# Kernel tuning notes

Hardware: AMD Instinct MI355X
Metric: run time of the kernel (lower is better)

The kernel has to match this reference:

```python
import jax, jax.numpy as jnp
import numpy as np

N, E, B = 25000, 400000, 64
IN, HID, OUT, EDGE, TDIM, L = 16, 128, 16, 16, 64, 4
EIN = 2 * HID + 1 + EDGE  # 273


def _sinusoidal(t, dim):
    half = dim // 2
    freqs = jnp.exp(jnp.arange(half, dtype=jnp.float32) * (-np.log(10000.0) / (half - 1)))
    a = t[:, None] * freqs[None, :]
    return jnp.concatenate([jnp.sin(a), jnp.cos(a)], axis=-1)


def _layernorm(h, g, b, eps=1e-5):
    mu = h.mean(-1, keepdims=True)
    v = h.var(-1, keepdims=True)
    return (h - mu) / jnp.sqrt(v + eps) * g + b


def setup_inputs() -> dict:
    key = jax.random.key(0)
    ks = iter(jax.random.split(key, 64))

    def rn(shape, scale=0.05):
        return jax.random.normal(next(ks), shape, dtype=jnp.float32) * scale

    inp = {
        'h': jax.random.normal(next(ks), (N, IN), dtype=jnp.float32),
        'x': jax.random.normal(next(ks), (N, 3), dtype=jnp.float32),
        'edge_index': jax.random.randint(next(ks), (2, E), 0, N),
        't': jax.random.uniform(next(ks), (B,), dtype=jnp.float32) * 1000.0,
        'edge_attr': jax.random.normal(next(ks), (E, EDGE), dtype=jnp.float32),
        'batch': jnp.sort(jax.random.randint(next(ks), (N,), 0, B)),
        # embeddings
        'node_w': rn((IN, HID)), 'node_b': jnp.zeros((HID,), jnp.float32),
        'tw1': rn((TDIM, HID)), 'tb1': jnp.zeros((HID,), jnp.float32),
        'tw2': rn((HID, HID)), 'tb2': jnp.zeros((HID,), jnp.float32),
        # per-layer stacked params (L, ...)
        'edge_w1': rn((L, EIN, HID)), 'edge_b1': jnp.zeros((L, HID), jnp.float32),
        'edge_w2': rn((L, HID, HID)), 'edge_b2': jnp.zeros((L, HID), jnp.float32),
        'att_w': rn((L, HID, 1)), 'att_b': jnp.zeros((L, 1), jnp.float32),
        'cw1': rn((L, HID, HID)), 'cb1': jnp.zeros((L, HID), jnp.float32),
        'cw2': rn((L, HID, 1), scale=0.001),  # xavier gain=0.001
        'nw1': rn((L, 2 * HID, HID)), 'nb1': jnp.zeros((L, HID), jnp.float32),
        'nw2': rn((L, HID, HID)), 'nb2': jnp.zeros((L, HID), jnp.float32),
        'ln_g': jnp.ones((L, HID), jnp.float32), 'ln_b': jnp.zeros((L, HID), jnp.float32),
        # heads
        'out_w1': rn((HID, HID)), 'out_b1': jnp.zeros((HID,), jnp.float32),
        'out_w2': rn((HID, OUT)), 'out_b2': jnp.zeros((OUT,), jnp.float32),
        'head_w': rn((HID, 3), scale=0.01), 'head_b': jnp.zeros((3,), jnp.float32),
    }
    return inp


def reference(h, x, edge_index, t, edge_attr, batch,
              node_w, node_b, tw1, tb1, tw2, tb2,
              edge_w1, edge_b1, edge_w2, edge_b2, att_w, att_b,
              cw1, cb1, cw2, nw1, nb1, nw2, nb2, ln_g, ln_b,
              out_w1, out_b1, out_w2, out_b2, head_w, head_b):
    silu = jax.nn.silu
    n_nodes = h.shape[0]
    row, col = edge_index[0], edge_index[1]

    # node + time embedding
    h = h @ node_w + node_b
    te = _sinusoidal(t, TDIM)
    te = silu(te @ tw1 + tb1) @ tw2 + tb2
    h = h + te[batch]

    for i in range(L):
        coord_diff = x[row] - x[col]                      # (E, 3)
        radial = (coord_diff ** 2).sum(-1, keepdims=True)  # (E, 1)
        edge_in = jnp.concatenate([h[row], h[col], radial, edge_attr], axis=-1)
        m = silu(silu(edge_in @ edge_w1[i] + edge_b1[i]) @ edge_w2[i] + edge_b2[i])
        att = jax.nn.sigmoid(m @ att_w[i] + att_b[i])
        m = m * att
        cw = silu(m @ cw1[i] + cb1[i]) @ cw2[i]           # (E, 1)
        coord_diff = coord_diff / jnp.sqrt(radial + 1e-8)  # normalize=True
        x = x + jax.ops.segment_sum(coord_diff * cw, row, num_segments=n_nodes)
        m_i = jax.ops.segment_sum(m, row, num_segments=n_nodes)
        h_in = jnp.concatenate([h, m_i], axis=-1)
        h_new = h + (silu(h_in @ nw1[i] + nb1[i]) @ nw2[i] + nb2[i])
        h = _layernorm(h_new, ln_g[i], ln_b[i])

    h_out = silu(h @ out_w1 + out_b1) @ out_w2 + out_b2  # (N, OUT)
    x_out = h @ head_w + head_b                           # (N, 3)
    return h_out, x_out
```

## Files before the change

### kernel.cpp

```cpp
#include <hip/hip_runtime.h>
#include <hip/hip_bf16.h>
#include <cmath>

#define NN      25000
#define NEDGE   400000
#define NBATCH  64
#define IN_DIM  16
#define HID     128
#define OUT_DIM 16
#define EDGE_DIM 16
#define TDIM    64
#define NL      4
#define EIN     273
#define EPB     64
#define W1KB    36
#define W2KB    16
#define A_PAD   65
#define A3OFF   (16*A_PAD*8)
#define NPB     32
#define NPAD    33

typedef short bfrag __attribute__((ext_vector_type(8)));
typedef float ffrag __attribute__((ext_vector_type(4)));

__device__ __forceinline__ float siluf(float v) { return v / (1.f + __expf(-v)); }
__device__ __forceinline__ float sigm(float v)  { return 1.f / (1.f + __expf(-v)); }
__device__ __forceinline__ unsigned short f2b(float f) {
    unsigned u = __float_as_uint(f);
    u = (u + 0x7FFFu + ((u >> 16) & 1u)) >> 16;
    return (unsigned short)u;
}
__device__ __forceinline__ float b2f(unsigned short b) {
    return __uint_as_float(((unsigned)b) << 16);
}
__device__ __forceinline__ int ileave(int n) {
    return (n & 0x60) | ((n & 15) << 1) | ((n >> 4) & 1);
}

__global__ __launch_bounds__(256) void hist_kernel(const int* __restrict__ row, int* __restrict__ deg) {
    const int tid = blockIdx.x * 256 + threadIdx.x;
    if (tid < NEDGE) atomicAdd(&deg[row[tid]], 1);
}

__global__ __launch_bounds__(1024) void scan_kernel(const int* __restrict__ deg, int* __restrict__ row_start) {
    __shared__ int part[1024];
    const int tid = threadIdx.x;
    const int base = tid * 25;
    int sum = 0;
    for (int i = 0; i < 25; i++) { const int idx = base + i; if (idx < NN) sum += deg[idx]; }
    part[tid] = sum;
    __syncthreads();
    for (int off = 1; off < 1024; off <<= 1) {
        int v = (tid >= off) ? part[tid - off] : 0;
        __syncthreads();
        part[tid] += v;
        __syncthreads();
    }
    int run = part[tid] - sum;
    for (int i = 0; i < 25; i++) {
        const int idx = base + i;
        if (idx < NN) { row_start[idx] = run; run += deg[idx]; }
    }
    if (tid == 1023) row_start[NN] = part[1023];
}

__global__ __launch_bounds__(256) void scatter_kernel(
    const int* __restrict__ row, const int* __restrict__ col,
    const int* __restrict__ row_start, int* __restrict__ cursor,
    int* __restrict__ rowp, int* __restrict__ colp, int* __restrict__ eorder)
{
    const int tid = blockIdx.x * 256 + threadIdx.x;
    if (tid >= NEDGE) return;
    const int r = row[tid];
    const int pos = row_start[r] + atomicAdd(&cursor[r], 1);
    rowp[pos] = r; colp[pos] = col[tid]; eorder[pos] = tid;
}

__global__ __launch_bounds__(256) void ea_pack(
    const float* __restrict__ ea, const int* __restrict__ eorder, unsigned short* __restrict__ eabp)
{
    const int tid = blockIdx.x * 256 + threadIdx.x;
    if (tid >= NEDGE) return;
    const int e = eorder[tid];
    const float4* src = (const float4*)&ea[(size_t)e * 16];
    bfrag o0, o1;
    #pragma unroll
    for (int q = 0; q < 2; q++) {
        const float4 a = src[q];
        o0[q*4+0] = (short)f2b(a.x); o0[q*4+1] = (short)f2b(a.y);
        o0[q*4+2] = (short)f2b(a.z); o0[q*4+3] = (short)f2b(a.w);
    }
    #pragma unroll
    for (int q = 0; q < 2; q++) {
        const float4 a = src[2+q];
        o1[q*4+0] = (short)f2b(a.x); o1[q*4+1] = (short)f2b(a.y);
        o1[q*4+2] = (short)f2b(a.z); o1[q*4+3] = (short)f2b(a.w);
    }
    *(bfrag*)&eabp[(size_t)tid * 16]     = o0;
    *(bfrag*)&eabp[(size_t)tid * 16 + 8] = o1;
}

__global__ __launch_bounds__(256) void prep_w(
    const float* __restrict__ ew1, const float* __restrict__ ew2, const float* __restrict__ cw1,
    unsigned short* __restrict__ w1p, unsigned short* __restrict__ w2p, unsigned short* __restrict__ c1p)
{
    const int PER_L = 68 * 128;
    int tid = blockIdx.x * 256 + threadIdx.x;
    if (tid >= NL * PER_L) return;
    const int l = tid / PER_L, rem = tid % PER_L;
    const int kb = rem >> 7, n = rem & 127;
    unsigned short o[8];
    if (kb < W1KB) {
        const float* W = ew1 + (size_t)l * EIN * HID;
        const int nc = ileave(n);
        #pragma unroll
        for (int j = 0; j < 8; j++) {
            const int k = kb * 8 + j;
            const int ok = (k < 256) ? k : (k < 272 ? k + 1 : (k == 272 ? 256 : -1));
            o[j] = (ok >= 0) ? f2b(W[(size_t)ok * HID + nc]) : (unsigned short)0;
        }
        #pragma unroll
        for (int j = 0; j < 8; j++) w1p[(((size_t)l * W1KB + kb) * 128 + n) * 8 + j] = o[j];
    } else if (kb < W1KB + W2KB) {
        const int kb2 = kb - W1KB;
        const float* W = ew2 + (size_t)l * HID * HID;
        const int nc = ileave(n);
        #pragma unroll
        for (int j = 0; j < 8; j++) o[j] = f2b(W[(size_t)(kb2 * 8 + j) * HID + nc]);
        #pragma unroll
        for (int j = 0; j < 8; j++) w2p[(((size_t)l * W2KB + kb2) * 128 + n) * 8 + j] = o[j];
    } else {
        const int kb2 = kb - W1KB - W2KB;
        const float* W = cw1 + (size_t)l * HID * HID;
        #pragma unroll
        for (int j = 0; j < 8; j++) o[j] = f2b(W[(size_t)(kb2 * 8 + j) * HID + n]);
        #pragma unroll
        for (int j = 0; j < 8; j++) c1p[(((size_t)l * W2KB + kb2) * 128 + n) * 8 + j] = o[j];
    }
}

__global__ __launch_bounds__(256) void prep_w2(
    const float* __restrict__ nw1, const float* __restrict__ nw2,
    const float* __restrict__ ow1, const float* __restrict__ ow2,
    unsigned short* __restrict__ n1p, unsigned short* __restrict__ n2p,
    unsigned short* __restrict__ o1p, unsigned short* __restrict__ o2p)
{
    const int C1 = NL * 32 * 128;
    const int C2 = C1 + NL * 16 * 128;
    const int C3 = C2 + 16 * 128;
    const int C4 = C3 + 16 * 16;
    int tid = blockIdx.x * 256 + threadIdx.x;
    if (tid >= C4) return;
    if (tid < C1) {
        const int l = tid / (32*128), rem = tid % (32*128);
        const int kb = rem >> 7, n = rem & 127;
        const int nc = ileave(n);
        #pragma unroll
        for (int j = 0; j < 8; j++)
            n1p[(size_t)tid*8 + j] = f2b(nw1[((size_t)l*256 + kb*8 + j)*128 + nc]);
    } else if (tid < C2) {
        const int t2 = tid - C1;
        const int l = t2 / (16*128), rem = t2 % (16*128);
        const int kb = rem >> 7, n = rem & 127;
        const int nc = ileave(n);
        #pragma unroll
        for (int j = 0; j < 8; j++)
            n2p[(size_t)t2*8 + j] = f2b(nw2[((size_t)l*128 + kb*8 + j)*128 + nc]);
    } else if (tid < C3) {
        const int t2 = tid - C2;
        const int kb = t2 >> 7, n = t2 & 127;
        #pragma unroll
        for (int j = 0; j < 8; j++)
            o1p[(size_t)t2*8 + j] = f2b(ow1[(size_t)(kb*8 + j)*128 + n]);
    } else {
        const int t2 = tid - C3;
        const int kb = t2 >> 4, n = t2 & 15;
        #pragma unroll
        for (int j = 0; j < 8; j++)
            o2p[(size_t)t2*8 + j] = f2b(ow2[(size_t)(kb*8 + j)*16 + n]);
    }
}

__global__ __launch_bounds__(HID) void te_kernel(
    const float* __restrict__ t, const float* __restrict__ tw1, const float* __restrict__ tb1,
    const float* __restrict__ tw2, const float* __restrict__ tb2, float* __restrict__ te_out)
{
    __shared__ float s0[TDIM];
    __shared__ float s1[HID];
    const int b = blockIdx.x, j = threadIdx.x;
    const float tv = t[b];
    if (j < TDIM) {
        const int k = j & 31;
        const float freq = expf((float)k * (-logf(10000.f) / 31.f));
        const float a = tv * freq;
        s0[j] = (j < 32) ? sinf(a) : cosf(a);
    }
    __syncthreads();
    float acc = tb1[j];
    for (int k = 0; k < TDIM; k++) acc += s0[k] * tw1[k*HID + j];
    s1[j] = siluf(acc);
    __syncthreads();
    float acc2 = tb2[j];
    for (int k = 0; k < HID; k++) acc2 += s1[k] * tw2[k*HID + j];
    te_out[b*HID + j] = acc2;
}

__global__ __launch_bounds__(HID) void embed_kernel(
    const float* __restrict__ h_in, const float* __restrict__ x_in,
    const int* __restrict__ batch,
    const float* __restrict__ node_w, const float* __restrict__ node_b,
    const float* __restrict__ te, float* __restrict__ h, unsigned short* __restrict__ hbf,
    float* __restrict__ x0)
{
    __shared__ float hs[IN_DIM];
    const int n = blockIdx.x, j = threadIdx.x;
    if (j < IN_DIM) hs[j] = h_in[n*IN_DIM + j];
    if (j >= 64 && j < 67) x0[n*3 + (j - 64)] = x_in[n*3 + (j - 64)];
    __syncthreads();
    float acc = node_b[j];
    #pragma unroll
    for (int k = 0; k < IN_DIM; k++) acc += hs[k] * node_w[k*HID + j];
    acc += te[batch[n]*HID + j];
    h[n*HID + j]   = acc;
    hbf[n*HID + j] = f2b(acc);
}

__global__ __launch_bounds__(256) void edge_mfma(
    const unsigned short* __restrict__ hbf, const float* __restrict__ x,
    float* __restrict__ x_new, float* __restrict__ m_i,
    const int* __restrict__ rowp, const int* __restrict__ colp,
    const unsigned short* __restrict__ eabp,
    const unsigned short* __restrict__ W1p, const float* __restrict__ B1,
    const unsigned short* __restrict__ W2p, const float* __restrict__ B2,
    const unsigned short* __restrict__ C1p, const float* __restrict__ CB1,
    const float* __restrict__ AW, const float* __restrict__ ABv,
    const float* __restrict__ CW2)
{
    __shared__ unsigned short sA[W1KB * A_PAD * 8];
    __shared__ int rc[EPB][2];
    __shared__ float AWs[HID];
    float* scr   = (float*)sA;
    float* attS  = scr;
    float* cpart = scr + 64;

    const int t = threadIdx.x;
    const int e0 = blockIdx.x * EPB;
    const int lane = t & 63, w = t >> 6;
    const int quad = lane >> 4, colid = lane & 15;

    float cd0 = 0.f, cd1 = 0.f, cd2 = 0.f;
    if (t < EPB) {
        const int r = rowp[e0 + t], c = colp[e0 + t];
        rc[t][0] = r; rc[t][1] = c;
        const float dx = x[r*3+0] - x[c*3+0];
        const float dy = x[r*3+1] - x[c*3+1];
        const float dz = x[r*3+2] - x[c*3+2];
        const float rad = dx*dx + dy*dy + dz*dz;
        const float inv = 1.f / sqrtf(rad + 1e-8f);
        cd0 = dx*inv; cd1 = dy*inv; cd2 = dz*inv;
        unsigned short* p34 = &sA[(34*A_PAD + t) * 8];
        p34[0] = f2b(rad);
        #pragma unroll
        for (int j = 1; j < 8; j++) p34[j] = 0;
        unsigned short* p35 = &sA[(35*A_PAD + t) * 8];
        #pragma unroll
        for (int j = 0; j < 8; j++) p35[j] = 0;
    }
    if (t >= 128 && t < 256) AWs[t - 128] = AW[t - 128];
    if (t < 128) {
        const int e = t >> 1, hh = t & 1;
        *(bfrag*)&sA[((32 + hh)*A_PAD + e) * 8] = *(const bfrag*)&eabp[(size_t)(e0 + e) * 16 + hh * 8];
    }
    __syncthreads();
    #pragma unroll
    for (int it = 0; it < 8; it++) {
        const int c = t + it * 256;
        const int e = (c >> 4) & 63;
        const int half = c >> 10;
        const int kb16 = c & 15;
        const int node = rc[e][half];
        *(bfrag*)&sA[((half*16 + kb16)*A_PAD + e) * 8] = *(const bfrag*)&hbf[(size_t)node * HID + kb16 * 8];
    }
    __syncthreads();

    ffrag acc1[4][2] = {};
    for (int ks = 0; ks < 9; ks++) {
        const int kb = ks * 4 + quad;
        const bfrag b0 = *(const bfrag*)&W1p[((size_t)kb * 128 + w*32 + colid) * 8];
        const bfrag b1 = *(const bfrag*)&W1p[((size_t)kb * 128 + w*32 + 16 + colid) * 8];
        #pragma unroll
        for (int mt = 0; mt < 4; mt++) {
            const bfrag a = *(const bfrag*)&sA[(kb*A_PAD + mt*16 + colid) * 8];
            acc1[mt][0] = __builtin_amdgcn_mfma_f32_16x16x32_bf16(a, b0, acc1[mt][0], 0, 0, 0);
            acc1[mt][1] = __builtin_amdgcn_mfma_f32_16x16x32_bf16(a, b1, acc1[mt][1], 0, 0, 0);
        }
    }
    __syncthreads();
    {
        const int f0 = w*32 + 2*colid;
        const int kb = f0 >> 3, j = f0 & 7;
        const float b0v = B1[f0], b1v = B1[f0+1];
        #pragma unroll
        for (int mt = 0; mt < 4; mt++)
            #pragma unroll
            for (int reg = 0; reg < 4; reg++) {
                const float v0 = siluf(acc1[mt][0][reg] + b0v);
                const float v1 = siluf(acc1[mt][1][reg] + b1v);
                const int e = mt*16 + quad*4 + reg;
                *(__hip_bfloat162*)&sA[(kb*A_PAD + e) * 8 + j] =
                    __float22bfloat162_rn(make_float2(v0, v1));
            }
    }
    __syncthreads();

    ffrag acc2[4][2] = {};
    for (int ks = 0; ks < 4; ks++) {
        const int kb = ks * 4 + quad;
        const bfrag b0 = *(const bfrag*)&W2p[((size_t)kb * 128 + w*32 + colid) * 8];
        const bfrag b1 = *(const bfrag*)&W2p[((size_t)kb * 128 + w*32 + 16 + colid) * 8];
        #pragma unroll
        for (int mt = 0; mt < 4; mt++) {
            const bfrag a = *(const bfrag*)&sA[(kb*A_PAD + mt*16 + colid) * 8];
            acc2[mt][0] = __builtin_amdgcn_mfma_f32_16x16x32_bf16(a, b0, acc2[mt][0], 0, 0, 0);
            acc2[mt][1] = __builtin_amdgcn_mfma_f32_16x16x32_bf16(a, b1, acc2[mt][1], 0, 0, 0);
        }
    }
    {
        const int f0 = w*32 + 2*colid;
        const int kb = f0 >> 3, j = f0 & 7;
        const float b0v = B2[f0], b1v = B2[f0+1];
        #pragma unroll
        for (int mt = 0; mt < 4; mt++)
            #pragma unroll
            for (int reg = 0; reg < 4; reg++) {
                const float v0 = siluf(acc2[mt][0][reg] + b0v);
                const float v1 = siluf(acc2[mt][1][reg] + b1v);
                const int e = mt*16 + quad*4 + reg;
                *(__hip_bfloat162*)&sA[A3OFF + (kb*A_PAD + e) * 8 + j] =
                    __float22bfloat162_rn(make_float2(v0, v1));
            }
    }
    __syncthreads();

    {
        const int e = t >> 2, q = t & 3;
        float s = 0.f;
        #pragma unroll
        for (int kk = 0; kk < 4; kk++) {
            const int kb = q*4 + kk;
            const bfrag v = *(const bfrag*)&sA[A3OFF + (kb*A_PAD + e) * 8];
            #pragma unroll
            for (int j = 0; j < 8; j++) s += b2f((unsigned short)v[j]) * AWs[kb*8 + j];
        }
        s += __shfl_xor(s, 1);
        s += __shfl_xor(s, 2);
        if (q == 0) attS[e] = sigm(s + ABv[0]);
    }
    __syncthreads();

    ffrag acc3[4][2] = {};
    for (int ks = 0; ks < 4; ks++) {
        const int kb = ks * 4 + quad;
        const bfrag b0 = *(const bfrag*)&C1p[((size_t)kb * 128 + w*32 + colid) * 8];
        const bfrag b1 = *(const bfrag*)&C1p[((size_t)kb * 128 + w*32 + 16 + colid) * 8];
        #pragma unroll
        for (int mt = 0; mt < 4; mt++) {
            const bfrag a = *(const bfrag*)&sA[A3OFF + (kb*A_PAD + mt*16 + colid) * 8];
            acc3[mt][0] = __builtin_amdgcn_mfma_f32_16x16x32_bf16(a, b0, acc3[mt][0], 0, 0, 0);
            acc3[mt][1] = __builtin_amdgcn_mfma_f32_16x16x32_bf16(a, b1, acc3[mt][1], 0, 0, 0);
        }
    }

    {
        const int fkb0 = lane >> 3,     fj = lane & 7;
        const int fkb1 = 8 + (lane >> 3);
        float a0 = 0.f, a1 = 0.f;
        for (int i = 0; i < 16; i++) {
            const int e = (w << 4) + i;
            const float av = attS[e];
            const int r = rc[e][0];
            a0 += b2f(sA[A3OFF + (fkb0*A_PAD + e) * 8 + fj]) * av;
            a1 += b2f(sA[A3OFF + (fkb1*A_PAD + e) * 8 + fj]) * av;
            const bool flush = (i == 15) || (rc[e+1][0] != r);
            if (flush) {
                atomicAdd(&m_i[(size_t)r * HID + lane],      a0);
                atomicAdd(&m_i[(size_t)r * HID + lane + 64], a1);
                a0 = 0.f; a1 = 0.f;
            }
        }
    }

    {
        const float cb0v = CB1[w*32 + colid], cb1v = CB1[w*32 + 16 + colid];
        const float cwv0 = CW2[w*32 + colid], cwv1 = CW2[w*32 + 16 + colid];
        float att_r[4][4];
        #pragma unroll
        for (int mt = 0; mt < 4; mt++) {
            const float4 a4 = *(const float4*)&attS[mt*16 + quad*4];
            att_r[mt][0] = a4.x; att_r[mt][1] = a4.y; att_r[mt][2] = a4.z; att_r[mt][3] = a4.w;
        }
        float p[4][4];
        #pragma unroll
        for (int mt = 0; mt < 4; mt++)
            #pragma unroll
            for (int reg = 0; reg < 4; reg++) p[mt][reg] = 0.f;
        #pragma unroll
        for (int mt = 0; mt < 4; mt++)
            #pragma unroll
            for (int nt = 0; nt < 2; nt++) {
                const float cb = nt ? cb1v : cb0v;
                const float cw = nt ? cwv1 : cwv0;
                #pragma unroll
                for (int reg = 0; reg < 4; reg++)
                    p[mt][reg] += siluf(att_r[mt][reg] * acc3[mt][nt][reg] + cb) * cw;
            }
        __syncthreads();
        #pragma unroll
        for (int mt = 0; mt < 4; mt++)
            #pragma unroll
            for (int reg = 0; reg < 4; reg++) {
                float s = p[mt][reg];
                s += __shfl_xor(s, 1);
                s += __shfl_xor(s, 2);
                s += __shfl_xor(s, 4);
                s += __shfl_xor(s, 8);
                if (colid == 0) cpart[(mt*16 + quad*4 + reg) * 4 + w] = s;
            }
    }
    __syncthreads();
    if (t < EPB) {
        const float s = cpart[t*4+0] + cpart[t*4+1] + cpart[t*4+2] + cpart[t*4+3];
        const int r = rc[t][0];
        atomicAdd(&x_new[r*3+0], cd0 * s);
        atomicAdd(&x_new[r*3+1], cd1 * s);
        atomicAdd(&x_new[r*3+2], cd2 * s);
    }
}

__global__ __launch_bounds__(256) void node_mfma(
    float* __restrict__ h, unsigned short* __restrict__ hbf, const float* __restrict__ m_i,
    const unsigned short* __restrict__ N1p, const float* __restrict__ NB1,
    const unsigned short* __restrict__ N2p, const float* __restrict__ NB2,
    const float* __restrict__ LG, const float* __restrict__ LB)
{
    __shared__ unsigned short sA[32 * NPAD * 8];
    __shared__ float mu_s[NPB], rs_s[NPB];
    float* hres = (float*)sA;

    const int t = threadIdx.x, lane = t & 63, w = t >> 6;
    const int quad = lane >> 4, colid = lane & 15;
    const int n0 = blockIdx.x * NPB;

    #pragma unroll
    for (int it = 0; it < 2; it++) {
        const int c = t + it * 256;
        const int e = c >> 4, kb = c & 15;
        const int nidx = min(n0 + e, NN - 1);
        *(bfrag*)&sA[(kb*NPAD + e) * 8] = *(const bfrag*)&hbf[(size_t)nidx * HID + kb * 8];
    }
    #pragma unroll
    for (int it = 0; it < 2; it++) {
        const int c = t + it * 256;
        const int e = c >> 4, kb = c & 15;
        const int nidx = min(n0 + e, NN - 1);
        const float4 v0 = *(const float4*)&m_i[(size_t)nidx * HID + kb * 8];
        const float4 v1 = *(const float4*)&m_i[(size_t)nidx * HID + kb * 8 + 4];
        bfrag bv;
        bv[0]=(short)f2b(v0.x); bv[1]=(short)f2b(v0.y); bv[2]=(short)f2b(v0.z); bv[3]=(short)f2b(v0.w);
        bv[4]=(short)f2b(v1.x); bv[5]=(short)f2b(v1.y); bv[6]=(short)f2b(v1.z); bv[7]=(short)f2b(v1.w);
        *(bfrag*)&sA[((16 + kb)*NPAD + e) * 8] = bv;
    }
    __syncthreads();

    ffrag acc1[2][2] = {};
    for (int ks = 0; ks < 8; ks++) {
        const int kb = ks * 4 + quad;
        const bfrag b0 = *(const bfrag*)&N1p[((size_t)kb * 128 + w*32 + colid) * 8];
        const bfrag b1 = *(const bfrag*)&N1p[((size_t)kb * 128 + w*32 + 16 + colid) * 8];
        #pragma unroll
        for (int mt = 0; mt < 2; mt++) {
            const bfrag a = *(const bfrag*)&sA[(kb*NPAD + mt*16 + colid) * 8];
            acc1[mt][0] = __builtin_amdgcn_mfma_f32_16x16x32_bf16(a, b0, acc1[mt][0], 0, 0, 0);
            acc1[mt][1] = __builtin_amdgcn_mfma_f32_16x16x32_bf16(a, b1, acc1[mt][1], 0, 0, 0);
        }
    }
    __syncthreads();
    {
        const int f0 = w*32 + 2*colid;
        const int kb = f0 >> 3, j = f0 & 7;
        const float b0v = NB1[f0], b1v = NB1[f0+1];
        #pragma unroll
        for (int mt = 0; mt < 2; mt++)
            #pragma unroll
            for (int reg = 0; reg < 4; reg++) {
                const float v0 = siluf(acc1[mt][0][reg] + b0v);
                const float v1 = siluf(acc1[mt][1][reg] + b1v);
                const int e = mt*16 + quad*4 + reg;
                *(__hip_bfloat162*)&sA[(kb*NPAD + e) * 8 + j] =
                    __float22bfloat162_rn(make_float2(v0, v1));
            }
    }
    __syncthreads();

    ffrag acc2[2][2] = {};
    for (int ks = 0; ks < 4; ks++) {
        const int kb = ks * 4 + quad;
        const bfrag b0 = *(const bfrag*)&N2p[((size_t)kb * 128 + w*32 + colid) * 8];
        const bfrag b1 = *(const bfrag*)&N2p[((size_t)kb * 128 + w*32 + 16 + colid) * 8];
        #pragma unroll
        for (int mt = 0; mt < 2; mt++) {
            const bfrag a = *(const bfrag*)&sA[(kb*NPAD + mt*16 + colid) * 8];
            acc2[mt][0] = __builtin_amdgcn_mfma_f32_16x16x32_bf16(a, b0, acc2[mt][0], 0, 0, 0);
            acc2[mt][1] = __builtin_amdgcn_mfma_f32_16x16x32_bf16(a, b1, acc2[mt][1], 0, 0, 0);
        }
    }
    __syncthreads();
    {
        const int f0 = w*32 + 2*colid;
        const float b0v = NB2[f0], b1v = NB2[f0+1];
        #pragma unroll
        for (int mt = 0; mt < 2; mt++)
            #pragma unroll
            for (int reg = 0; reg < 4; reg++) {
                const int row = mt*16 + quad*4 + reg;
                const int nidx = min(n0 + row, NN - 1);
                const float2 hr = *(const float2*)&h[(size_t)nidx*HID + f0];
                float2 o;
                o.x = acc2[mt][0][reg] + b0v + hr.x;
                o.y = acc2[mt][1][reg] + b1v + hr.y;
                *(float2*)&hres[row*130 + f0] = o;
            }
    }
    __syncthreads();
    {
        const int row = t >> 3, q = t & 7;
        float s = 0.f, s2 = 0.f;
        #pragma unroll
        for (int i = 0; i < 16; i++) {
            const float v = hres[row*130 + q*16 + i];
            s += v; s2 += v*v;
        }
        s += __shfl_xor(s, 1); s2 += __shfl_xor(s2, 1);
        s += __shfl_xor(s, 2); s2 += __shfl_xor(s2, 2);
        s += __shfl_xor(s, 4); s2 += __shfl_xor(s2, 4);
        if (q == 0) {
            const float mu = s * (1.f/HID);
            mu_s[row] = mu;
            rs_s[row] = rsqrtf(s2 * (1.f/HID) - mu*mu + 1e-5f);
        }
    }
    __syncthreads();
    for (int idx = t; idx < NPB*HID; idx += 256) {
        const int row = idx >> 7, f = idx & 127;
        const int n = n0 + row;
        if (n < NN) {
            const float v = (hres[row*130 + f] - mu_s[row]) * rs_s[row] * LG[f] + LB[f];
            h[(size_t)n*HID + f]   = v;
            hbf[(size_t)n*HID + f] = f2b(v);
        }
    }
}

__global__ __launch_bounds__(256) void out_mfma(
    const unsigned short* __restrict__ hbf,
    const unsigned short* __restrict__ O1p, const float* __restrict__ OB1,
    const unsigned short* __restrict__ O2p, const float* __restrict__ OB2,
    const float* __restrict__ HW, const float* __restrict__ HB,
    float* __restrict__ out)
{
    __shared__ unsigned short sA[32 * A_PAD * 8];
    __shared__ float hws[HID*3];
    const int A2O = 16 * A_PAD * 8;

    const int t = threadIdx.x, lane = t & 63, w = t >> 6;
    const int quad = lane >> 4, colid = lane & 15;
    const int n0 = blockIdx.x * 64;

    if (t < 128)      { hws[t] = HW[t]; hws[t+128] = HW[t+128]; }
    else if (t < 256) { const int i = t - 128 + 256; if (i < 384) hws[i] = HW[i]; }
    #pragma unroll
    for (int it = 0; it < 4; it++) {
        const int c = t + it * 256;
        const int e = c >> 4, kb = c & 15;
        const int nidx = min(n0 + e, NN - 1);
        *(bfrag*)&sA[(kb*A_PAD + e) * 8] = *(const bfrag*)&hbf[(size_t)nidx * HID + kb * 8];
    }
    __syncthreads();

    ffrag acc1[4][2] = {};
    for (int ks = 0; ks < 4; ks++) {
        const int kb = ks * 4 + quad;
        const bfrag b0 = *(const bfrag*)&O1p[((size_t)kb * 128 + w*32 + colid) * 8];
        const bfrag b1 = *(const bfrag*)&O1p[((size_t)kb * 128 + w*32 + 16 + colid) * 8];
        #pragma unroll
        for (int mt = 0; mt < 4; mt++) {
            const bfrag a = *(const bfrag*)&sA[(kb*A_PAD + mt*16 + colid) * 8];
            acc1[mt][0] = __builtin_amdgcn_mfma_f32_16x16x32_bf16(a, b0, acc1[mt][0], 0, 0, 0);
            acc1[mt][1] = __builtin_amdgcn_mfma_f32_16x16x32_bf16(a, b1, acc1[mt][1], 0, 0, 0);
        }
    }
    {
        const float bias0 = OB1[w*32 + colid], bias1 = OB1[w*32 + 16 + colid];
        #pragma unroll
        for (int mt = 0; mt < 4; mt++)
            #pragma unroll
            for (int nt = 0; nt < 2; nt++) {
                const float bb = nt ? bias1 : bias0;
                const int f = w*32 + nt*16 + colid;
                const int kb = f >> 3, j = f & 7;
                #pragma unroll
                for (int reg = 0; reg < 4; reg++) {
                    const float v = siluf(acc1[mt][nt][reg] + bb);
                    const int e = mt*16 + quad*4 + reg;
                    sA[A2O + (kb*A_PAD + e) * 8 + j] = f2b(v);
                }
            }
    }
    __syncthreads();

    ffrag acco = {};
    for (int ks = 0; ks < 4; ks++) {
        const int kb = ks * 4 + quad;
        const bfrag a = *(const bfrag*)&sA[A2O + (kb*A_PAD + w*16 + colid) * 8];
        const bfrag b = *(const bfrag*)&O2p[((size_t)kb * 16 + colid) * 8];
        acco = __builtin_amdgcn_mfma_f32_16x16x32_bf16(a, b, acco, 0, 0, 0);
    }
    #pragma unroll
    for (int reg = 0; reg < 4; reg++) {
        const int rowg = w*16 + quad*4 + reg;
        const int n = n0 + rowg;
        if (n < NN) out[(size_t)n*OUT_DIM + colid] = acco[reg] + OB2[colid];
    }

    {
        const int rloc = t >> 2, q = t & 3;
        float s0 = 0.f, s1 = 0.f, s2 = 0.f;
        #pragma unroll
        for (int kk = 0; kk < 4; kk++) {
            const int kb = q*4 + kk;
            const bfrag v = *(const bfrag*)&sA[(kb*A_PAD + rloc) * 8];
            #pragma unroll
            for (int j = 0; j < 8; j++) {
                const float hv = b2f((unsigned short)v[j]);
                const int k = kb*8 + j;
                s0 += hv * hws[k*3+0]; s1 += hv * hws[k*3+1]; s2 += hv * hws[k*3+2];
            }
        }
        s0 += __shfl_xor(s0, 1); s1 += __shfl_xor(s1, 1); s2 += __shfl_xor(s2, 1);
        s0 += __shfl_xor(s0, 2); s1 += __shfl_xor(s1, 2); s2 += __shfl_xor(s2, 2);
        const int n = n0 + rloc;
        if (q == 0 && n < NN) {
            out[(size_t)NN*OUT_DIM + n*3 + 0] = s0 + HB[0];
            out[(size_t)NN*OUT_DIM + n*3 + 1] = s1 + HB[1];
            out[(size_t)NN*OUT_DIM + n*3 + 2] = s2 + HB[2];
        }
    }
}

extern "C" void kernel_launch(void* const* d_in, const int* in_sizes, int n_in,
                              void* d_out, int out_size, void* d_ws, size_t ws_size,
                              hipStream_t stream) {
    (void)in_sizes; (void)n_in; (void)out_size; (void)ws_size;
    const float* h_in      = (const float*)d_in[0];
    const float* x_in      = (const float*)d_in[1];
    const int*   edge_idx  = (const int*)  d_in[2];
    const float* t         = (const float*)d_in[3];
    const float* edge_attr = (const float*)d_in[4];
    const int*   batch     = (const int*)  d_in[5];
    const float* node_w = (const float*)d_in[6];
    const float* node_b = (const float*)d_in[7];
    const float* tw1    = (const float*)d_in[8];
    const float* tb1    = (const float*)d_in[9];
    const float* tw2    = (const float*)d_in[10];
    const float* tb2    = (const float*)d_in[11];
    const float* ew1    = (const float*)d_in[12];
    const float* eb1    = (const float*)d_in[13];
    const float* ew2    = (const float*)d_in[14];
    const float* eb2    = (const float*)d_in[15];
    const float* attw   = (const float*)d_in[16];
    const float* attb   = (const float*)d_in[17];
    const float* cw1    = (const float*)d_in[18];
    const float* cb1    = (const float*)d_in[19];
    const float* cw2    = (const float*)d_in[20];
    const float* nw1    = (const float*)d_in[21];
    const float* nb1    = (const float*)d_in[22];
    const float* nw2    = (const float*)d_in[23];
    const float* nb2    = (const float*)d_in[24];
    const float* lng    = (const float*)d_in[25];
    const float* lnb    = (const float*)d_in[26];
    const float* ow1    = (const float*)d_in[27];
    const float* ob1    = (const float*)d_in[28];
    const float* ow2    = (const float*)d_in[29];
    const float* ob2    = (const float*)d_in[30];
    const float* hw     = (const float*)d_in[31];
    const float* hb     = (const float*)d_in[32];

    const int* row = edge_idx;
    const int* col = edge_idx + NEDGE;

    float* ws  = (float*)d_ws;
    float* te  = ws;
    float* h   = te  + NBATCH*HID;
    float* m_i = h   + (size_t)NN*HID;
    float* x0  = m_i + (size_t)NN*HID;
    float* x1  = x0  + NN*3;
    unsigned short* hbf  = (unsigned short*)(x1 + NN*3);
    unsigned short* eabp = hbf + (size_t)NN*HID;
    unsigned short* w1p  = eabp + (size_t)NEDGE*EDGE_DIM;
    unsigned short* w2p  = w1p + (size_t)NL*W1KB*128*8;
    unsigned short* c1p  = w2p + (size_t)NL*W2KB*128*8;
    unsigned short* n1p  = c1p + (size_t)NL*W2KB*128*8;
    unsigned short* n2p  = n1p + (size_t)NL*32*128*8;
    unsigned short* o1p  = n2p + (size_t)NL*16*128*8;
    unsigned short* o2p  = o1p + (size_t)16*128*8;
    int* deg       = (int*)(o2p + 16*16*8);
    int* row_start = deg + NN;
    int* cursor    = row_start + NN + 1;
    int* rowp      = cursor + NN;
    int* colp      = rowp + NEDGE;
    int* eorder    = colp + NEDGE;

    hipMemsetAsync(deg, 0, NN*sizeof(int), stream);
    hipMemsetAsync(cursor, 0, NN*sizeof(int), stream);
    hist_kernel<<<(NEDGE+255)/256, 256, 0, stream>>>(row, deg);
    scan_kernel<<<1, 1024, 0, stream>>>(deg, row_start);
    scatter_kernel<<<(NEDGE+255)/256, 256, 0, stream>>>(row, col, row_start, cursor, rowp, colp, eorder);
    ea_pack<<<(NEDGE+255)/256, 256, 0, stream>>>(edge_attr, eorder, eabp);

    prep_w<<<(NL*68*128 + 255)/256, 256, 0, stream>>>(ew1, ew2, cw1, w1p, w2p, c1p);
    prep_w2<<<(NL*32*128 + NL*16*128 + 16*128 + 16*16 + 255)/256, 256, 0, stream>>>(
        nw1, nw2, ow1, ow2, n1p, n2p, o1p, o2p);
    te_kernel<<<NBATCH, HID, 0, stream>>>(t, tw1, tb1, tw2, tb2, te);
    embed_kernel<<<NN, HID, 0, stream>>>(h_in, x_in, batch, node_w, node_b, te, h, hbf, x0);

    const int NBLK = (NN + NPB - 1) / NPB;
    const int OBLK = (NN + 63) / 64;
    float* xc = x0; float* xn = x1;
    for (int i = 0; i < NL; i++) {
        hipMemsetAsync(m_i, 0, (size_t)NN*HID*sizeof(float), stream);
        hipMemcpyAsync(xn, xc, (size_t)NN*3*sizeof(float), hipMemcpyDeviceToDevice, stream);
        edge_mfma<<<NEDGE/EPB, 256, 0, stream>>>(
            hbf, xc, xn, m_i, rowp, colp, eabp,
            w1p + (size_t)i*W1KB*128*8, eb1 + (size_t)i*HID,
            w2p + (size_t)i*W2KB*128*8, eb2 + (size_t)i*HID,
            c1p + (size_t)i*W2KB*128*8, cb1 + (size_t)i*HID,
            attw + (size_t)i*HID, attb + i,
            cw2 + (size_t)i*HID);
        node_mfma<<<NBLK, 256, 0, stream>>>(
            h, hbf, m_i,
            n1p + (size_t)i*32*128*8, nb1 + (size_t)i*HID,
            n2p + (size_t)i*16*128*8, nb2 + (size_t)i*HID,
            lng + (size_t)i*HID,      lnb + (size_t)i*HID);
        float* tmp = xc; xc = xn; xn = tmp;
    }

    out_mfma<<<OBLK, 256, 0, stream>>>(hbf, o1p, ob1, o2p, ob2, hw, hb, (float*)d_out);
}
```

Before: 1.083 ms.

## Fold biases into MFMA accumulators, compute attention via MFMA, fuse m_i zeroing

```diff
diff --git a/kernel.cpp b/kernel.cpp
--- a/kernel.cpp
+++ b/kernel.cpp
@@ -102,9 +102,11 @@
 
 __global__ __launch_bounds__(256) void prep_w(
     const float* __restrict__ ew1, const float* __restrict__ ew2, const float* __restrict__ cw1,
-    unsigned short* __restrict__ w1p, unsigned short* __restrict__ w2p, unsigned short* __restrict__ c1p)
-{
-    const int PER_L = 68 * 128;
+    const float* __restrict__ attw,
+    unsigned short* __restrict__ w1p, unsigned short* __restrict__ w2p,
+    unsigned short* __restrict__ c1p, unsigned short* __restrict__ awp)
+{
+    const int PER_L = 70 * 128;
     int tid = blockIdx.x * 256 + threadIdx.x;
     if (tid >= NL * PER_L) return;
     const int l = tid / PER_L, rem = tid % PER_L;
@@ -129,13 +131,22 @@
         for (int j = 0; j < 8; j++) o[j] = f2b(W[(size_t)(kb2 * 8 + j) * HID + nc]);
         #pragma unroll
         for (int j = 0; j < 8; j++) w2p[(((size_t)l * W2KB + kb2) * 128 + n) * 8 + j] = o[j];
-    } else {
+    } else if (kb < W1KB + 2*W2KB) {
         const int kb2 = kb - W1KB - W2KB;
         const float* W = cw1 + (size_t)l * HID * HID;
         #pragma unroll
         for (int j = 0; j < 8; j++) o[j] = f2b(W[(size_t)(kb2 * 8 + j) * HID + n]);
         #pragma unroll
         for (int j = 0; j < 8; j++) c1p[(((size_t)l * W2KB + kb2) * 128 + n) * 8 + j] = o[j];
+    } else {
+        const int kbp = kb - W1KB - 2*W2KB;
+        const int kbA = kbp * 8 + (n >> 4);
+        const int colv = n & 15;
+        const float* AWl = attw + (size_t)l * HID;
+        #pragma unroll
+        for (int j = 0; j < 8; j++) o[j] = f2b(AWl[kbA*8 + j]);
+        #pragma unroll
+        for (int j = 0; j < 8; j++) awp[(((size_t)l * 16 + kbA) * 16 + colv) * 8 + j] = o[j];
     }
 }
 
@@ -205,24 +216,27 @@
     te_out[b*HID + j] = acc2;
 }
 
-__global__ __launch_bounds__(HID) void embed_kernel(
+__global__ __launch_bounds__(256) void embed_kernel(
     const float* __restrict__ h_in, const float* __restrict__ x_in,
     const int* __restrict__ batch,
     const float* __restrict__ node_w, const float* __restrict__ node_b,
     const float* __restrict__ te, float* __restrict__ h, unsigned short* __restrict__ hbf,
-    float* __restrict__ x0)
-{
-    __shared__ float hs[IN_DIM];
-    const int n = blockIdx.x, j = threadIdx.x;
-    if (j < IN_DIM) hs[j] = h_in[n*IN_DIM + j];
+    float* __restrict__ x0, float* __restrict__ m_i)
+{
+    __shared__ float hs[2][IN_DIM];
+    const int local = threadIdx.x >> 7;
+    const int j = threadIdx.x & 127;
+    const int n = blockIdx.x * 2 + local;
+    if (j < IN_DIM) hs[local][j] = h_in[n*IN_DIM + j];
     if (j >= 64 && j < 67) x0[n*3 + (j - 64)] = x_in[n*3 + (j - 64)];
     __syncthreads();
     float acc = node_b[j];
     #pragma unroll
-    for (int k = 0; k < IN_DIM; k++) acc += hs[k] * node_w[k*HID + j];
+    for (int k = 0; k < IN_DIM; k++) acc += hs[local][k] * node_w[k*HID + j];
     acc += te[batch[n]*HID + j];
-    h[n*HID + j]   = acc;
-    hbf[n*HID + j] = f2b(acc);
+    h[(size_t)n*HID + j]   = acc;
+    hbf[(size_t)n*HID + j] = f2b(acc);
+    m_i[(size_t)n*HID + j] = 0.f;
 }
 
 __global__ __launch_bounds__(256) void edge_mfma(
@@ -233,15 +247,13 @@
     const unsigned short* __restrict__ W1p, const float* __restrict__ B1,
     const unsigned short* __restrict__ W2p, const float* __restrict__ B2,
     const unsigned short* __restrict__ C1p, const float* __restrict__ CB1,
-    const float* __restrict__ AW, const float* __restrict__ ABv,
+    const unsigned short* __restrict__ AWp, const float* __restrict__ ABv,
     const float* __restrict__ CW2)
 {
     __shared__ unsigned short sA[W1KB * A_PAD * 8];
     __shared__ int rc[EPB][2];
-    __shared__ float AWs[HID];
-    float* scr   = (float*)sA;
-    float* attS  = scr;
-    float* cpart = scr + 64;
+    float* attS = (float*)sA;
+    float* pscr = (float*)&sA[A3OFF];
 
     const int t = threadIdx.x;
     const int e0 = blockIdx.x * EPB;
@@ -266,7 +278,6 @@
         #pragma unroll
         for (int j = 0; j < 8; j++) p35[j] = 0;
     }
-    if (t >= 128 && t < 256) AWs[t - 128] = AW[t - 128];
     if (t < 128) {
         const int e = t >> 1, hh = t & 1;
         *(bfrag*)&sA[((32 + hh)*A_PAD + e) * 8] = *(const bfrag*)&eabp[(size_t)(e0 + e) * 16 + hh * 8];
@@ -283,7 +294,15 @@
     }
     __syncthreads();
 
-    ffrag acc1[4][2] = {};
+    const int f0 = w*32 + 2*colid;
+    ffrag acc1[4][2];
+    {
+        const float b0v = B1[f0], b1v = B1[f0+1];
+        #pragma unroll
+        for (int mt = 0; mt < 4; mt++)
+            #pragma unroll
+            for (int r = 0; r < 4; r++) { acc1[mt][0][r] = b0v; acc1[mt][1][r] = b1v; }
+    }
     for (int ks = 0; ks < 9; ks++) {
         const int kb = ks * 4 + quad;
         const bfrag b0 = *(const bfrag*)&W1p[((size_t)kb * 128 + w*32 + colid) * 8];
@@ -297,15 +316,13 @@
     }
     __syncthreads();
     {
-        const int f0 = w*32 + 2*colid;
         const int kb = f0 >> 3, j = f0 & 7;
-        const float b0v = B1[f0], b1v = B1[f0+1];
         #pragma unroll
         for (int mt = 0; mt < 4; mt++)
             #pragma unroll
             for (int reg = 0; reg < 4; reg++) {
-                const float v0 = siluf(acc1[mt][0][reg] + b0v);
-                const float v1 = siluf(acc1[mt][1][reg] + b1v);
+                const float v0 = siluf(acc1[mt][0][reg]);
+                const float v1 = siluf(acc1[mt][1][reg]);
                 const int e = mt*16 + quad*4 + reg;
                 *(__hip_bfloat162*)&sA[(kb*A_PAD + e) * 8 + j] =
                     __float22bfloat162_rn(make_float2(v0, v1));
@@ -313,7 +330,14 @@
     }
     __syncthreads();
 
-    ffrag acc2[4][2] = {};
+    ffrag acc2[4][2];
+    {
+        const float b0v = B2[f0], b1v = B2[f0+1];
+        #pragma unroll
+        for (int mt = 0; mt < 4; mt++)
+            #pragma unroll
+            for (int r = 0; r < 4; r++) { acc2[mt][0][r] = b0v; acc2[mt][1][r] = b1v; }
+    }
     for (int ks = 0; ks < 4; ks++) {
         const int kb = ks * 4 + quad;
         const bfrag b0 = *(const bfrag*)&W2p[((size_t)kb * 128 + w*32 + colid) * 8];
@@ -326,15 +350,13 @@
         }
     }
     {
-        const int f0 = w*32 + 2*colid;
         const int kb = f0 >> 3, j = f0 & 7;
-        const float b0v = B2[f0], b1v = B2[f0+1];
         #pragma unroll
         for (int mt = 0; mt < 4; mt++)
             #pragma unroll
             for (int reg = 0; reg < 4; reg++) {
-                const float v0 = siluf(acc2[mt][0][reg] + b0v);
-                const float v1 = siluf(acc2[mt][1][reg] + b1v);
+                const float v0 = siluf(acc2[mt][0][reg]);
+                const float v1 = siluf(acc2[mt][1][reg]);
                 const int e = mt*16 + quad*4 + reg;
                 *(__hip_bfloat162*)&sA[A3OFF + (kb*A_PAD + e) * 8 + j] =
                     __float22bfloat162_rn(make_float2(v0, v1));
@@ -342,34 +364,35 @@
     }
     __syncthreads();
 
-    {
-        const int e = t >> 2, q = t & 3;
-        float s = 0.f;
-        #pragma unroll
-        for (int kk = 0; kk < 4; kk++) {
-            const int kb = q*4 + kk;
-            const bfrag v = *(const bfrag*)&sA[A3OFF + (kb*A_PAD + e) * 8];
-            #pragma unroll
-            for (int j = 0; j < 8; j++) s += b2f((unsigned short)v[j]) * AWs[kb*8 + j];
-        }
-        s += __shfl_xor(s, 1);
-        s += __shfl_xor(s, 2);
-        if (q == 0) attS[e] = sigm(s + ABv[0]);
-    }
-    __syncthreads();
-
+    ffrag accA;
+    {
+        const float abv = ABv[0];
+        #pragma unroll
+        for (int r = 0; r < 4; r++) accA[r] = abv;
+    }
     ffrag acc3[4][2] = {};
     for (int ks = 0; ks < 4; ks++) {
         const int kb = ks * 4 + quad;
-        const bfrag b0 = *(const bfrag*)&C1p[((size_t)kb * 128 + w*32 + colid) * 8];
-        const bfrag b1 = *(const bfrag*)&C1p[((size_t)kb * 128 + w*32 + 16 + colid) * 8];
+        const bfrag ab = *(const bfrag*)&AWp[((size_t)kb * 16 + colid) * 8];
+        const bfrag c0 = *(const bfrag*)&C1p[((size_t)kb * 128 + w*32 + colid) * 8];
+        const bfrag c1 = *(const bfrag*)&C1p[((size_t)kb * 128 + w*32 + 16 + colid) * 8];
+        const bfrag aw_frag = *(const bfrag*)&sA[A3OFF + (kb*A_PAD + w*16 + colid) * 8];
+        accA = __builtin_amdgcn_mfma_f32_16x16x32_bf16(aw_frag, ab, accA, 0, 0, 0);
         #pragma unroll
         for (int mt = 0; mt < 4; mt++) {
-            const bfrag a = *(const bfrag*)&sA[A3OFF + (kb*A_PAD + mt*16 + colid) * 8];
-            acc3[mt][0] = __builtin_amdgcn_mfma_f32_16x16x32_bf16(a, b0, acc3[mt][0], 0, 0, 0);
-            acc3[mt][1] = __builtin_amdgcn_mfma_f32_16x16x32_bf16(a, b1, acc3[mt][1], 0, 0, 0);
-        }
-    }
+            const bfrag a = (mt == w) ? aw_frag
+                : *(const bfrag*)&sA[A3OFF + (kb*A_PAD + mt*16 + colid) * 8];
+            acc3[mt][0] = __builtin_amdgcn_mfma_f32_16x16x32_bf16(a, c0, acc3[mt][0], 0, 0, 0);
+            acc3[mt][1] = __builtin_amdgcn_mfma_f32_16x16x32_bf16(a, c1, acc3[mt][1], 0, 0, 0);
+        }
+    }
+    if (colid == 0) {
+        #pragma unroll
+        for (int reg = 0; reg < 4; reg++) attS[w*16 + quad*4 + reg] = accA[reg];
+    }
+    __syncthreads();
+    if (t < EPB) attS[t] = sigm(attS[t]);
+    __syncthreads();
 
     {
         const int fkb0 = lane >> 3,     fj = lane & 7;
@@ -390,46 +413,35 @@
         }
     }
 
+    float p[4][4];
     {
         const float cb0v = CB1[w*32 + colid], cb1v = CB1[w*32 + 16 + colid];
         const float cwv0 = CW2[w*32 + colid], cwv1 = CW2[w*32 + 16 + colid];
-        float att_r[4][4];
         #pragma unroll
         for (int mt = 0; mt < 4; mt++) {
             const float4 a4 = *(const float4*)&attS[mt*16 + quad*4];
-            att_r[mt][0] = a4.x; att_r[mt][1] = a4.y; att_r[mt][2] = a4.z; att_r[mt][3] = a4.w;
-        }
-        float p[4][4];
-        #pragma unroll
-        for (int mt = 0; mt < 4; mt++)
-            #pragma unroll
-            for (int reg = 0; reg < 4; reg++) p[mt][reg] = 0.f;
-        #pragma unroll
-        for (int mt = 0; mt < 4; mt++)
-            #pragma unroll
-            for (int nt = 0; nt < 2; nt++) {
-                const float cb = nt ? cb1v : cb0v;
-                const float cw = nt ? cwv1 : cwv0;
-                #pragma unroll
-                for (int reg = 0; reg < 4; reg++)
-                    p[mt][reg] += siluf(att_r[mt][reg] * acc3[mt][nt][reg] + cb) * cw;
-            }
-        __syncthreads();
-        #pragma unroll
-        for (int mt = 0; mt < 4; mt++)
-            #pragma unroll
-            for (int reg = 0; reg < 4; reg++) {
-                float s = p[mt][reg];
-                s += __shfl_xor(s, 1);
-                s += __shfl_xor(s, 2);
-                s += __shfl_xor(s, 4);
-                s += __shfl_xor(s, 8);
-                if (colid == 0) cpart[(mt*16 + quad*4 + reg) * 4 + w] = s;
-            }
-    }
+            const float att_r[4] = {a4.x, a4.y, a4.z, a4.w};
+            #pragma unroll
+            for (int reg = 0; reg < 4; reg++)
+                p[mt][reg] = siluf(att_r[reg] * acc3[mt][0][reg] + cb0v) * cwv0
+                           + siluf(att_r[reg] * acc3[mt][1][reg] + cb1v) * cwv1;
+        }
+    }
+    __syncthreads();
+    #pragma unroll
+    for (int mt = 0; mt < 4; mt++)
+        #pragma unroll
+        for (int reg = 0; reg < 4; reg++)
+            pscr[(mt*16 + quad*4 + reg)*68 + w*16 + colid] = p[mt][reg];
     __syncthreads();
     if (t < EPB) {
-        const float s = cpart[t*4+0] + cpart[t*4+1] + cpart[t*4+2] + cpart[t*4+3];
+        const float* pr = pscr + t*68;
+        float s = 0.f;
+        #pragma unroll
+        for (int k2 = 0; k2 < 16; k2++) {
+            const float4 v = *(const float4*)&pr[k2*4];
+            s += (v.x + v.y) + (v.z + v.w);
+        }
         const int r = rc[t][0];
         atomicAdd(&x_new[r*3+0], cd0 * s);
         atomicAdd(&x_new[r*3+1], cd1 * s);
@@ -438,7 +450,7 @@
 }
 
 __global__ __launch_bounds__(256) void node_mfma(
-    float* __restrict__ h, unsigned short* __restrict__ hbf, const float* __restrict__ m_i,
+    float* __restrict__ h, unsigned short* __restrict__ hbf, float* __restrict__ m_i,
     const unsigned short* __restrict__ N1p, const float* __restrict__ NB1,
     const unsigned short* __restrict__ N2p, const float* __restrict__ NB2,
     const float* __restrict__ LG, const float* __restrict__ LB)
@@ -469,10 +481,23 @@
         bv[0]=(short)f2b(v0.x); bv[1]=(short)f2b(v0.y); bv[2]=(short)f2b(v0.z); bv[3]=(short)f2b(v0.w);
         bv[4]=(short)f2b(v1.x); bv[5]=(short)f2b(v1.y); bv[6]=(short)f2b(v1.z); bv[7]=(short)f2b(v1.w);
         *(bfrag*)&sA[((16 + kb)*NPAD + e) * 8] = bv;
-    }
-    __syncthreads();
-
-    ffrag acc1[2][2] = {};
+        if (n0 + e < NN) {
+            const float4 z4 = {0.f, 0.f, 0.f, 0.f};
+            *(float4*)&m_i[(size_t)nidx * HID + kb * 8]     = z4;
+            *(float4*)&m_i[(size_t)nidx * HID + kb * 8 + 4] = z4;
+        }
+    }
+    __syncthreads();
+
+    const int f0 = w*32 + 2*colid;
+    ffrag acc1[2][2];
+    {
+        const float b0v = NB1[f0], b1v = NB1[f0+1];
+        #pragma unroll
+        for (int mt = 0; mt < 2; mt++)
+            #pragma unroll
+            for (int r = 0; r < 4; r++) { acc1[mt][0][r] = b0v; acc1[mt][1][r] = b1v; }
+    }
     for (int ks = 0; ks < 8; ks++) {
         const int kb = ks * 4 + quad;
         const bfrag b0 = *(const bfrag*)&N1p[((size_t)kb * 128 + w*32 + colid) * 8];
@@ -486,15 +511,13 @@
     }
     __syncthreads();
     {
-        const int f0 = w*32 + 2*colid;
         const int kb = f0 >> 3, j = f0 & 7;
-        const float b0v = NB1[f0], b1v = NB1[f0+1];
         #pragma unroll
         for (int mt = 0; mt < 2; mt++)
             #pragma unroll
             for (int reg = 0; reg < 4; reg++) {
-                const float v0 = siluf(acc1[mt][0][reg] + b0v);
-                const float v1 = siluf(acc1[mt][1][reg] + b1v);
+                const float v0 = siluf(acc1[mt][0][reg]);
+                const float v1 = siluf(acc1[mt][1][reg]);
                 const int e = mt*16 + quad*4 + reg;
                 *(__hip_bfloat162*)&sA[(kb*NPAD + e) * 8 + j] =
                     __float22bfloat162_rn(make_float2(v0, v1));
@@ -502,7 +525,14 @@
     }
     __syncthreads();
 
-    ffrag acc2[2][2] = {};
+    ffrag acc2[2][2];
+    {
+        const float b0v = NB2[f0], b1v = NB2[f0+1];
+        #pragma unroll
+        for (int mt = 0; mt < 2; mt++)
+            #pragma unroll
+            for (int r = 0; r < 4; r++) { acc2[mt][0][r] = b0v; acc2[mt][1][r] = b1v; }
+    }
     for (int ks = 0; ks < 4; ks++) {
         const int kb = ks * 4 + quad;
         const bfrag b0 = *(const bfrag*)&N2p[((size_t)kb * 128 + w*32 + colid) * 8];
@@ -516,8 +546,6 @@
     }
     __syncthreads();
     {
-        const int f0 = w*32 + 2*colid;
-        const float b0v = NB2[f0], b1v = NB2[f0+1];
         #pragma unroll
         for (int mt = 0; mt < 2; mt++)
             #pragma unroll
@@ -526,8 +554,8 @@
                 const int nidx = min(n0 + row, NN - 1);
                 const float2 hr = *(const float2*)&h[(size_t)nidx*HID + f0];
                 float2 o;
-                o.x = acc2[mt][0][reg] + b0v + hr.x;
-                o.y = acc2[mt][1][reg] + b1v + hr.y;
+                o.x = acc2[mt][0][reg] + hr.x;
+                o.y = acc2[mt][1][reg] + hr.y;
                 *(float2*)&hres[row*130 + f0] = o;
             }
     }
@@ -587,7 +615,14 @@
     }
     __syncthreads();
 
-    ffrag acc1[4][2] = {};
+    ffrag acc1[4][2];
+    {
+        const float b0v = OB1[w*32 + colid], b1v = OB1[w*32 + 16 + colid];
+        #pragma unroll
+        for (int mt = 0; mt < 4; mt++)
+            #pragma unroll
+            for (int r = 0; r < 4; r++) { acc1[mt][0][r] = b0v; acc1[mt][1][r] = b1v; }
+    }
     for (int ks = 0; ks < 4; ks++) {
         const int kb = ks * 4 + quad;
         const bfrag b0 = *(const bfrag*)&O1p[((size_t)kb * 128 + w*32 + colid) * 8];
@@ -600,17 +635,15 @@
         }
     }
     {
-        const float bias0 = OB1[w*32 + colid], bias1 = OB1[w*32 + 16 + colid];
         #pragma unroll
         for (int mt = 0; mt < 4; mt++)
             #pragma unroll
             for (int nt = 0; nt < 2; nt++) {
-                const float bb = nt ? bias1 : bias0;
                 const int f = w*32 + nt*16 + colid;
                 const int kb = f >> 3, j = f & 7;
                 #pragma unroll
                 for (int reg = 0; reg < 4; reg++) {
-                    const float v = siluf(acc1[mt][nt][reg] + bb);
+                    const float v = siluf(acc1[mt][nt][reg]);
                     const int e = mt*16 + quad*4 + reg;
                     sA[A2O + (kb*A_PAD + e) * 8 + j] = f2b(v);
                 }
@@ -618,7 +651,12 @@
     }
     __syncthreads();
 
-    ffrag acco = {};
+    ffrag acco;
+    {
+        const float ob2v = OB2[colid];
+        #pragma unroll
+        for (int r = 0; r < 4; r++) acco[r] = ob2v;
+    }
     for (int ks = 0; ks < 4; ks++) {
         const int kb = ks * 4 + quad;
         const bfrag a = *(const bfrag*)&sA[A2O + (kb*A_PAD + w*16 + colid) * 8];
@@ -629,7 +667,7 @@
     for (int reg = 0; reg < 4; reg++) {
         const int rowg = w*16 + quad*4 + reg;
         const int n = n0 + rowg;
-        if (n < NN) out[(size_t)n*OUT_DIM + colid] = acco[reg] + OB2[colid];
+        if (n < NN) out[(size_t)n*OUT_DIM + colid] = acco[reg];
     }
 
     {
@@ -713,7 +751,8 @@
     unsigned short* n2p  = n1p + (size_t)NL*32*128*8;
     unsigned short* o1p  = n2p + (size_t)NL*16*128*8;
     unsigned short* o2p  = o1p + (size_t)16*128*8;
-    int* deg       = (int*)(o2p + 16*16*8);
+    unsigned short* awp  = o2p + (size_t)16*16*8;
+    int* deg       = (int*)(awp + (size_t)NL*16*16*8);
     int* row_start = deg + NN;
     int* cursor    = row_start + NN + 1;
     int* rowp      = cursor + NN;
@@ -727,24 +766,23 @@
     scatter_kernel<<<(NEDGE+255)/256, 256, 0, stream>>>(row, col, row_start, cursor, rowp, colp, eorder);
     ea_pack<<<(NEDGE+255)/256, 256, 0, stream>>>(edge_attr, eorder, eabp);
 
-    prep_w<<<(NL*68*128 + 255)/256, 256, 0, stream>>>(ew1, ew2, cw1, w1p, w2p, c1p);
+    prep_w<<<(NL*70*128 + 255)/256, 256, 0, stream>>>(ew1, ew2, cw1, attw, w1p, w2p, c1p, awp);
     prep_w2<<<(NL*32*128 + NL*16*128 + 16*128 + 16*16 + 255)/256, 256, 0, stream>>>(
         nw1, nw2, ow1, ow2, n1p, n2p, o1p, o2p);
     te_kernel<<<NBATCH, HID, 0, stream>>>(t, tw1, tb1, tw2, tb2, te);
-    embed_kernel<<<NN, HID, 0, stream>>>(h_in, x_in, batch, node_w, node_b, te, h, hbf, x0);
+    embed_kernel<<<NN/2, 256, 0, stream>>>(h_in, x_in, batch, node_w, node_b, te, h, hbf, x0, m_i);
 
     const int NBLK = (NN + NPB - 1) / NPB;
     const int OBLK = (NN + 63) / 64;
     float* xc = x0; float* xn = x1;
     for (int i = 0; i < NL; i++) {
-        hipMemsetAsync(m_i, 0, (size_t)NN*HID*sizeof(float), stream);
         hipMemcpyAsync(xn, xc, (size_t)NN*3*sizeof(float), hipMemcpyDeviceToDevice, stream);
         edge_mfma<<<NEDGE/EPB, 256, 0, stream>>>(
             hbf, xc, xn, m_i, rowp, colp, eabp,
             w1p + (size_t)i*W1KB*128*8, eb1 + (size_t)i*HID,
             w2p + (size_t)i*W2KB*128*8, eb2 + (size_t)i*HID,
             c1p + (size_t)i*W2KB*128*8, cb1 + (size_t)i*HID,
-            attw + (size_t)i*HID, attb + i,
+            awp + (size_t)i*16*16*8, attb + i,
             cw2 + (size_t)i*HID);
         node_mfma<<<NBLK, 256, 0, stream>>>(
             h, hbf, m_i,
```

Measured after the change: 1.109 ms. 1.02x slower.
